# Kernel optimization log

Hardware: AMD Instinct MI355X
Metric: run time of the kernel (lower is better)

## Reference

```python
import jax, jax.numpy as jnp
import numpy as np

NUM_HEADS = 16
HEAD_DIM = 128
NUM_KV_HEADS = 8
NUM_KV_GROUPS = 2
HIDDEN = 2048
SCALE = 0.5  # hardcoded in the original SDPA call


def _fixed_sincos_pos(E, H):
    # matches ReusedProjReconstructor._fixed_sincos_pos (H even here)
    half = H // 2
    freq = jnp.exp(-jnp.log(jnp.float32(10000.0)) * jnp.arange(half, dtype=jnp.float32) / half)
    pos = jnp.arange(E, dtype=jnp.float32)[:, None]
    ang = pos * freq[None, :]
    return jnp.concatenate([jnp.sin(ang), jnp.cos(ang)], axis=1)  # [E, H]


def setup_inputs() -> dict:
    key = jax.random.key(0)
    ks = jax.random.split(key, 8)
    B, M, H = 4, 2048, HIDDEN
    kv_dim = NUM_KV_HEADS * HEAD_DIM
    s = 0.02
    return {
        "mem_act": jax.random.normal(ks[0], (B, M, H), jnp.float32),
        "Wq": jax.random.normal(ks[1], (H, H), jnp.float32) * s,
        "bq": jax.random.normal(ks[2], (H,), jnp.float32) * s,
        "Wk": jax.random.normal(ks[3], (kv_dim, H), jnp.float32) * s,
        "bk": jax.random.normal(ks[4], (kv_dim,), jnp.float32) * s,
        "Wv": jax.random.normal(ks[5], (kv_dim, H), jnp.float32) * s,
        "bv": jax.random.normal(ks[6], (kv_dim,), jnp.float32) * s,
        "Wo": jax.random.normal(ks[7], (H, H), jnp.float32) * s,
        "E": 2048,
    }


def reference(mem_act, Wq, bq, Wk, bk, Wv, bv, Wo, E):
    B, M, H = mem_act.shape
    # positional query hidden, shared across batch (q_ln is Identity)
    q_hidden = _fixed_sincos_pos(E, H).astype(mem_act.dtype)  # [E, H]
    q = (q_hidden @ Wq.T + bq).reshape(E, NUM_HEADS, HEAD_DIM)          # [E, nh, hd]
    k = (mem_act @ Wk.T + bk).reshape(B, M, NUM_KV_HEADS, HEAD_DIM)     # [B, M, nkv, hd]
    v = (mem_act @ Wv.T + bv).reshape(B, M, NUM_KV_HEADS, HEAD_DIM)
    # GQA: repeat kv heads (repeat_interleave over head dim)
    k = jnp.repeat(k, NUM_KV_GROUPS, axis=2)  # [B, M, nh, hd]
    v = jnp.repeat(v, NUM_KV_GROUPS, axis=2)
    # non-causal SDPA with scale=0.5, query broadcast over batch
    scores = jnp.einsum("ehd,bmhd->bhem", q, k) * SCALE  # [B, nh, E, M]
    attn = jax.nn.softmax(scores, axis=-1)
    out = jnp.einsum("bhem,bmhd->behd", attn, v).reshape(B, E, H)
    pred = out @ Wo.T  # o_proj (no bias, Qwen2 style)
    return pred
```

## Files before the change

### kernel.cpp

```cpp
#include <hip/hip_runtime.h>
#include <hip/hip_bf16.h>

typedef __attribute__((ext_vector_type(8))) short short8;
typedef __attribute__((ext_vector_type(4))) float f32x4;
typedef __attribute__((ext_vector_type(16))) float f32x16;
typedef unsigned short ushort_t;

__device__ __forceinline__ unsigned short f2bf(float x) {
    unsigned int u = __builtin_bit_cast(unsigned int, x);
    unsigned int r = (u + 0x7fffu + ((u >> 16) & 1u)) >> 16;
    return (unsigned short)r;
}

__device__ __forceinline__ void gload_lds16(const ushort_t* g, ushort_t* l) {
    __builtin_amdgcn_global_load_lds(
        (const __attribute__((address_space(1))) void*)g,
        (__attribute__((address_space(3))) void*)l, 16, 0, 0);
}

#define MFMA16(A, B, C) __builtin_amdgcn_mfma_f32_16x16x32_bf16((A), (B), (C), 0, 0, 0)
#define MFMA32(A, B, C) __builtin_amdgcn_mfma_f32_32x32x16_bf16((A), (B), (C), 0, 0, 0)

__global__ __launch_bounds__(256) void cvt_all(const float* __restrict__ im,
                                               const float* __restrict__ iq,
                                               const float* __restrict__ ik,
                                               const float* __restrict__ iv,
                                               const float* __restrict__ io,
                                               ushort_t* __restrict__ om,
                                               ushort_t* __restrict__ oq,
                                               ushort_t* __restrict__ ok,
                                               ushort_t* __restrict__ ov,
                                               ushort_t* __restrict__ oo) {
    long i = ((long)blockIdx.x * 256 + threadIdx.x) << 3;
    const float* s;
    ushort_t* d;
    if (i < 16777216)      { s = im + i;              d = om + i; }
    else if (i < 20971520) { s = iq + (i - 16777216); d = oq + (i - 16777216); }
    else if (i < 23068672) { s = ik + (i - 20971520); d = ok + (i - 20971520); }
    else if (i < 25165824) { s = iv + (i - 23068672); d = ov + (i - 23068672); }
    else                   { s = io + (i - 25165824); d = oo + (i - 25165824); }
    const float4* p = (const float4*)s;
    float4 a = p[0], b = p[1];
    short8 o;
    o[0] = (short)f2bf(a.x); o[1] = (short)f2bf(a.y);
    o[2] = (short)f2bf(a.z); o[3] = (short)f2bf(a.w);
    o[4] = (short)f2bf(b.x); o[5] = (short)f2bf(b.y);
    o[6] = (short)f2bf(b.z); o[7] = (short)f2bf(b.w);
    *(short8*)d = o;
}

__global__ __launch_bounds__(256) void fill_qh(ushort_t* __restrict__ qh) {
    int idx = blockIdx.x * 256 + threadIdx.x;
    int e = idx >> 10, i = idx & 1023;
    float freq = __expf(-9.2103403719761836f * (float)i * (1.0f / 1024.0f));
    float ang = (float)e * freq;
    qh[(size_t)e * 2048 + i]        = f2bf(sinf(ang));
    qh[(size_t)e * 2048 + 1024 + i] = f2bf(cosf(ang));
}

__global__ __launch_bounds__(256) void gemm_q(const ushort_t* __restrict__ A,
                                              const ushort_t* __restrict__ Bw,
                                              const float* __restrict__ bias,
                                              ushort_t* __restrict__ Cout,
                                              int M, int N, int K) {
    __shared__ ushort_t As[128 * 32];
    __shared__ ushort_t Bs[128 * 32];
    const int tid = threadIdx.x;
    const int lane = tid & 63;
    const int wid = tid >> 6;
    const int g = lane >> 4;
    const int r = lane & 15;
    const int wr = wid >> 1, wc = wid & 1;
    const int nbn = N >> 7;
    const int bm = blockIdx.x / nbn, bn = blockIdx.x % nbn;
    const int row0 = bm << 7, col0 = bn << 7;

    f32x4 acc[4][4];
#pragma unroll
    for (int i = 0; i < 4; ++i)
#pragma unroll
        for (int j = 0; j < 4; ++j) acc[i][j] = (f32x4){0.f, 0.f, 0.f, 0.f};

    const int f0 = tid * 8;
    const int r0_ = f0 >> 5, c0_ = f0 & 31;
    const int f1 = (256 + tid) * 8;
    const int r1_ = f1 >> 5, c1_ = f1 & 31;

    for (int k0 = 0; k0 < K; k0 += 32) {
        __syncthreads();
        gload_lds16(A  + (size_t)(row0 + r0_) * K + k0 + c0_, As + f0);
        gload_lds16(A  + (size_t)(row0 + r1_) * K + k0 + c1_, As + f1);
        gload_lds16(Bw + (size_t)(col0 + r0_) * K + k0 + c0_, Bs + f0);
        gload_lds16(Bw + (size_t)(col0 + r1_) * K + k0 + c1_, Bs + f1);
        __syncthreads();
        short8 af[4], bfr[4];
#pragma unroll
        for (int i = 0; i < 4; ++i) {
            af[i]  = *(const short8*)(As + (wr * 64 + i * 16 + r) * 32 + g * 8);
            bfr[i] = *(const short8*)(Bs + (wc * 64 + i * 16 + r) * 32 + g * 8);
        }
#pragma unroll
        for (int i = 0; i < 4; ++i)
#pragma unroll
            for (int j = 0; j < 4; ++j) acc[i][j] = MFMA16(af[i], bfr[j], acc[i][j]);
    }

#pragma unroll
    for (int j = 0; j < 4; ++j) {
        const int col = col0 + wc * 64 + j * 16 + r;
        const float bv = bias[col];
#pragma unroll
        for (int i = 0; i < 4; ++i) {
            const int rowb = row0 + wr * 64 + i * 16 + g * 4;
#pragma unroll
            for (int t = 0; t < 4; ++t) {
                float v = (acc[i][j][t] + bv) * 0.5f;
                Cout[(size_t)(rowb + t) * N + col] = f2bf(v);
            }
        }
    }
}

template <int EPI>
__global__ __launch_bounds__(512, 1) void gemm256(const ushort_t* __restrict__ A,
                                                  const ushort_t* __restrict__ Bw,
                                                  const float* __restrict__ b0,
                                                  const float* __restrict__ b1,
                                                  void* __restrict__ C0,
                                                  void* __restrict__ C1,
                                                  int M, int N, int K) {
    __shared__ ushort_t As[3][256 * 32];
    __shared__ ushort_t Bs[3][256 * 32];
    const int tid = threadIdx.x, lane = tid & 63;
    const int wid = tid >> 6;
    const int q5 = lane & 31, hi = lane >> 5;
    const int wm = wid >> 2, wn = wid & 3;
    const int nbn = N >> 8;
    const int nwg = gridDim.x;
    const int swz = (blockIdx.x & 7) * (nwg >> 3) + (blockIdx.x >> 3);
    const int bm = swz / nbn, bn = swz % nbn;
    const int row0 = bm << 8, col0 = bn << 8;
    const int NT = K >> 5;

    f32x16 acc[4][2];
#pragma unroll
    for (int mi = 0; mi < 4; ++mi)
#pragma unroll
        for (int nj = 0; nj < 2; ++nj)
#pragma unroll
            for (int rr = 0; rr < 16; ++rr) acc[mi][nj][rr] = 0.f;

    auto STAGE_HALF = [&](int buf, int kt, int i) {
        const int k0 = kt << 5;
        const int fb = (i * 512 + tid) << 4;
        const int rp = fb >> 7;
        const int bo = ((fb >> 4) & 7) ^ (rp & 7);
        const int row = rp * 2 + (bo >> 2);
        const int kc = (bo & 3) << 3;
        gload_lds16(A  + (size_t)(row0 + row) * K + k0 + kc, &As[buf][0] + (fb >> 1));
        gload_lds16(Bw + (size_t)(col0 + row) * K + k0 + kc, &Bs[buf][0] + (fb >> 1));
    };

    STAGE_HALF(0, 0, 0); STAGE_HALF(0, 0, 1);
    STAGE_HALF(1, 1, 0); STAGE_HALF(1, 1, 1);
    asm volatile("s_waitcnt vmcnt(4)" ::: "memory");
    __builtin_amdgcn_sched_barrier(0);
    __builtin_amdgcn_s_barrier();
    __builtin_amdgcn_sched_barrier(0);

    for (int t = 0; t < NT; ++t) {
        const int buf = t % 3;
        const char* Ab = (const char*)&As[buf][0];
        const char* Bb = (const char*)&Bs[buf][0];
#pragma unroll
        for (int ph = 0; ph < 2; ++ph) {
            short8 af[4], bfr[2];
#pragma unroll
            for (int nj = 0; nj < 2; ++nj) {
                const int col = wn * 64 + nj * 32 + q5;
                const int rp = col >> 1;
                const int blk = (((col & 1) << 2) + ph * 2 + hi) ^ (rp & 7);
                bfr[nj] = *(const short8*)(Bb + rp * 128 + blk * 16);
            }
#pragma unroll
            for (int mi = 0; mi < 4; ++mi) {
                const int row = wm * 128 + mi * 32 + q5;
                const int rp = row >> 1;
                const int blk = (((row & 1) << 2) + ph * 2 + hi) ^ (rp & 7);
                af[mi] = *(const short8*)(Ab + rp * 128 + blk * 16);
            }
            if (t + 2 < NT) STAGE_HALF((t + 2) % 3, t + 2, ph);
            __builtin_amdgcn_s_setprio(1);
#pragma unroll
            for (int mi = 0; mi < 4; ++mi)
#pragma unroll
                for (int nj = 0; nj < 2; ++nj)
                    acc[mi][nj] = MFMA32(af[mi], bfr[nj], acc[mi][nj]);
            __builtin_amdgcn_s_setprio(0);
            if (ph == 0) {
                __builtin_amdgcn_sched_barrier(0);
                __builtin_amdgcn_s_barrier();
                __builtin_amdgcn_sched_barrier(0);
            }
        }

        if (t + 2 < NT) {
            asm volatile("s_waitcnt vmcnt(4)" ::: "memory");
        } else if (t + 1 < NT) {
            asm volatile("s_waitcnt vmcnt(0)" ::: "memory");
        }
        if (t + 1 < NT) {
            __builtin_amdgcn_sched_barrier(0);
            __builtin_amdgcn_s_barrier();
            __builtin_amdgcn_sched_barrier(0);
        }
    }

#pragma unroll
    for (int mi = 0; mi < 4; ++mi)
#pragma unroll
        for (int nj = 0; nj < 2; ++nj) {
            const int col = col0 + wn * 64 + nj * 32 + q5;
            if (EPI == 2) {
                float* outp = (float*)C0;
#pragma unroll
                for (int rr = 0; rr < 16; ++rr) {
                    const int row = row0 + wm * 128 + mi * 32 + (rr & 3) + 8 * (rr >> 2) + 4 * hi;
                    outp[(size_t)row * N + col] = acc[mi][nj][rr];
                }
            } else {
                if (col < 1024) {
                    const float bv = b0[col];
                    ushort_t* Kp = (ushort_t*)C0;
#pragma unroll
                    for (int rr = 0; rr < 16; ++rr) {
                        const int row = row0 + wm * 128 + mi * 32 + (rr & 3) + 8 * (rr >> 2) + 4 * hi;
                        Kp[(size_t)row * 1024 + col] = f2bf(acc[mi][nj][rr] + bv);
                    }
                } else {
                    const int vcol = col - 1024;
                    const float bv = b1[vcol];
                    ushort_t* Vt = (ushort_t*)C1;
#pragma unroll
                    for (int G = 0; G < 4; ++G) {
                        const int m0 = row0 + wm * 128 + mi * 32 + G * 8 + 4 * hi;
                        const int bb = m0 >> 11;
                        const int mm = m0 & 2047;
                        const size_t vtrow = (size_t)(bb * 8 + (vcol >> 7)) * 128 + (vcol & 127);
                        unsigned int p0 = (unsigned int)f2bf(acc[mi][nj][G * 4 + 0] + bv)
                                        | ((unsigned int)f2bf(acc[mi][nj][G * 4 + 1] + bv) << 16);
                        unsigned int p1 = (unsigned int)f2bf(acc[mi][nj][G * 4 + 2] + bv)
                                        | ((unsigned int)f2bf(acc[mi][nj][G * 4 + 3] + bv) << 16);
                        uint2 pk; pk.x = p0; pk.y = p1;
                        *(uint2*)(Vt + vtrow * 2048 + mm) = pk;
                    }
                }
            }
        }
}

__global__ __launch_bounds__(512, 2) void attn_kernel(const ushort_t* __restrict__ Q,
                                                      const ushort_t* __restrict__ Kg,
                                                      const ushort_t* __restrict__ Vt,
                                                      ushort_t* __restrict__ O) {
    __shared__ ushort_t Ks[2][64 * 128];
    __shared__ ushort_t Vts[2][128 * 64];

    const int tid = threadIdx.x, lane = tid & 63, wid = tid >> 6;
    const int q5 = lane & 31;
    const int hi = lane >> 5;
    const int wq = wid & 3;
    const int wg = (blockIdx.x & 7) * 64 + (blockIdx.x >> 3);
    const int bkvh = wg >> 4;
    const int etile = wg & 15;
    const int b = bkvh >> 3, kvh = bkvh & 7;
    const int h = kvh * 2 + (wid >> 2);
    const int e0 = etile * 128;
    const int qrow = e0 + wq * 32 + q5;

    short8 Qf[8];
    {
        const ushort_t* qp = Q + (size_t)qrow * 2048 + h * 128 + hi * 8;
#pragma unroll
        for (int c = 0; c < 8; ++c) Qf[c] = *(const short8*)(qp + c * 16);
    }

    unsigned aK[2][8];
#pragma unroll
    for (int h2 = 0; h2 < 2; ++h2) {
        const int key = h2 * 32 + q5;
#pragma unroll
        for (int c = 0; c < 8; ++c)
            aK[h2][c] = key * 256 + (((c * 2 + hi) ^ (key & 7)) << 4);
    }
    unsigned aV[4];
#pragma unroll
    for (int c16 = 0; c16 < 4; ++c16)
        aV[c16] = q5 * 128 + (((c16 * 2 + hi) ^ (q5 & 7)) << 4);

    float lrow = 0.f;
    f32x16 oacc[4];
#pragma unroll
    for (int d0 = 0; d0 < 4; ++d0)
#pragma unroll
        for (int r = 0; r < 16; ++r) oacc[d0][r] = 0.f;

    f32x16 Z16;
#pragma unroll
    for (int r = 0; r < 16; ++r) Z16[r] = 0.f;

    const ushort_t* Kbase  = Kg + (size_t)b * 2048 * 1024 + kvh * 128;
    const ushort_t* Vtbase = Vt + (size_t)bkvh * 128 * 2048;

    auto STAGE = [&](int buf, int kv0) {
#pragma unroll
        for (int i = 0; i < 2; ++i) {
            const int fb = (i * 8 + wid) * 1024 + lane * 16;
            const int key = fb >> 8;
            const int blk = (fb >> 4) & 15;
            gload_lds16(Kbase + (size_t)(kv0 + key) * 1024 + ((blk ^ (key & 7)) << 3),
                        &Ks[buf][0] + (fb >> 1));
            const int d = fb >> 7;
            const int kb = (fb >> 4) & 7;
            gload_lds16(Vtbase + (size_t)d * 2048 + kv0 + ((kb ^ (d & 7)) << 3),
                        &Vts[buf][0] + (fb >> 1));
        }
    };

    auto TILE = [&](int bo) {
        f32x16 sS[2];
        __builtin_amdgcn_s_setprio(1);
#pragma unroll
        for (int c = 0; c < 8; ++c) {
            short8 ka0 = *(const short8*)((const char*)Ks + bo + aK[0][c]);
            short8 ka1 = *(const short8*)((const char*)Ks + bo + aK[1][c]);
            sS[0] = MFMA32(ka0, Qf[c], (c == 0) ? Z16 : sS[0]);
            sS[1] = MFMA32(ka1, Qf[c], (c == 0) ? Z16 : sS[1]);
        }
        __builtin_amdgcn_s_setprio(0);

#pragma unroll
        for (int h2 = 0; h2 < 2; ++h2)
#pragma unroll
            for (int r = 0; r < 16; ++r) sS[h2][r] = __expf(sS[h2][r]);

        float ts[16];
#pragma unroll
        for (int i = 0; i < 8; ++i) ts[i] = sS[0][2 * i] + sS[0][2 * i + 1];
#pragma unroll
        for (int i = 0; i < 8; ++i) ts[8 + i] = sS[1][2 * i] + sS[1][2 * i + 1];
#pragma unroll
        for (int s = 8; s > 0; s >>= 1)
#pragma unroll
            for (int i = 0; i < s; ++i) ts[i] += ts[i + s];
        lrow += ts[0] + __shfl_xor(ts[0], 32);

        unsigned int W[2][4][2];
#pragma unroll
        for (int h2 = 0; h2 < 2; ++h2)
#pragma unroll
            for (int q4 = 0; q4 < 4; ++q4)
#pragma unroll
                for (int p = 0; p < 2; ++p) {
                    unsigned int w;
                    asm("v_cvt_pk_bf16_f32 %0, %1, %2"
                        : "=v"(w)
                        : "v"(sS[h2][q4 * 4 + 2 * p]), "v"(sS[h2][q4 * 4 + 2 * p + 1]));
                    W[h2][q4][p] = w;
                }

#pragma unroll
        for (int c16 = 0; c16 < 4; ++c16) {
            const int h2 = c16 >> 1;
            const int q4a = (c16 & 1) * 2, q4b = q4a + 1;
            auto r0 = __builtin_amdgcn_permlane32_swap(W[h2][q4a][0], W[h2][q4b][0], false, false);
            auto r1 = __builtin_amdgcn_permlane32_swap(W[h2][q4a][1], W[h2][q4b][1], false, false);
            union { unsigned int w[4]; short8 v; } pa;
            pa.w[0] = r0[0];
            pa.w[1] = r1[0];
            pa.w[2] = r0[1];
            pa.w[3] = r1[1];
            __builtin_amdgcn_s_setprio(1);
#pragma unroll
            for (int d0 = 0; d0 < 4; ++d0) {
                short8 vb = *(const short8*)((const char*)Vts + bo + aV[c16] + d0 * 4096);
                oacc[d0] = MFMA32(pa.v, vb, oacc[d0]);
            }
            __builtin_amdgcn_s_setprio(0);
        }
    };

    STAGE(0, 0);
    __syncthreads();

#pragma unroll 1
    for (int tt = 0; tt < 16; ++tt) {
        STAGE(1, (2 * tt + 1) * 64);
        TILE(0);
        __syncthreads();
        if (tt < 15) STAGE(0, (2 * tt + 2) * 64);
        TILE(16384);
        __syncthreads();
    }

#pragma unroll
    for (int reg = 0; reg < 16; ++reg) {
        const int qr = (reg & 3) + 8 * (reg >> 2) + 4 * hi;
        const float lr = __shfl(lrow, qr);
        const float inv = 1.0f / lr;
        const int e = e0 + wq * 32 + qr;
        ushort_t* op = O + ((size_t)b * 2048 + e) * 2048 + h * 128 + q5;
#pragma unroll
        for (int d0 = 0; d0 < 4; ++d0)
            op[d0 * 32] = f2bf(oacc[d0][reg] * inv);
    }
}

extern "C" void kernel_launch(void* const* d_in, const int* in_sizes, int n_in,
                              void* d_out, int out_size, void* d_ws, size_t ws_size,
                              hipStream_t stream) {
    const float* mem_act = (const float*)d_in[0];
    const float* Wq = (const float*)d_in[1];
    const float* bq = (const float*)d_in[2];
    const float* Wk = (const float*)d_in[3];
    const float* bk = (const float*)d_in[4];
    const float* Wv = (const float*)d_in[5];
    const float* bv = (const float*)d_in[6];
    const float* Wo = (const float*)d_in[7];
    float* out = (float*)d_out;

    char* w = (char*)d_ws;
    ushort_t* memb = (ushort_t*)w; w += (size_t)16777216 * 2;
    ushort_t* wqb  = (ushort_t*)w; w += (size_t)4194304 * 2;
    ushort_t* wkvb = (ushort_t*)w; w += (size_t)4194304 * 2;
    ushort_t* wob  = (ushort_t*)w; w += (size_t)4194304 * 2;
    ushort_t* qh   = (ushort_t*)w; w += (size_t)4194304 * 2;
    ushort_t* Qp   = (ushort_t*)w; w += (size_t)4194304 * 2;
    ushort_t* Kp   = (ushort_t*)w; w += (size_t)8388608 * 2;
    ushort_t* Vtp  = (ushort_t*)w; w += (size_t)8388608 * 2;
    ushort_t* AO   = (ushort_t*)w; w += (size_t)16777216 * 2;

    dim3 blk(256);
    cvt_all<<<14336, blk, 0, stream>>>(mem_act, Wq, Wk, Wv, Wo,
                                       memb, wqb, wkvb, wkvb + (size_t)2097152, wob);
    fill_qh<<<(2048 * 1024) / 256, blk, 0, stream>>>(qh);

    gemm_q<<<16 * 16, blk, 0, stream>>>(qh, wqb, bq, Qp, 2048, 2048, 2048);

    gemm256<0><<<256, dim3(512), 0, stream>>>(memb, wkvb, bk, bv, Kp, Vtp, 8192, 2048, 2048);

    attn_kernel<<<512, dim3(512), 0, stream>>>(Qp, Kp, Vtp, AO);

    gemm256<2><<<256, dim3(512), 0, stream>>>(AO, wob, nullptr, nullptr, out, nullptr, 8192, 2048, 2048);
}
```

Before: 373.4 us.

## Shrink GEMM tiles to 256x128 with double buffering and fuse prep kernels

The large GEMMs move from 256x256 tiles with 512 threads, a triple-buffered LDS ring and one block per CU to 256x128 tiles with 256 threads, double buffering and up to three blocks per CU, launched as 512 blocks. The aim is more resident waves and better latency hiding across blocks, and with 256 CUs the doubled block count should fill the device better. In exchange the loads and barriers are coarser: each k-step waits for all loads with vmcnt(0). The fp32-to-bf16 conversion and sincos query fill are also merged into one launch to save a kernel launch.

```diff
diff --git a/kernel.cpp b/kernel.cpp
--- a/kernel.cpp
+++ b/kernel.cpp
@@ -21,41 +21,43 @@
 #define MFMA16(A, B, C) __builtin_amdgcn_mfma_f32_16x16x32_bf16((A), (B), (C), 0, 0, 0)
 #define MFMA32(A, B, C) __builtin_amdgcn_mfma_f32_32x32x16_bf16((A), (B), (C), 0, 0, 0)
 
-__global__ __launch_bounds__(256) void cvt_all(const float* __restrict__ im,
-                                               const float* __restrict__ iq,
-                                               const float* __restrict__ ik,
-                                               const float* __restrict__ iv,
-                                               const float* __restrict__ io,
-                                               ushort_t* __restrict__ om,
-                                               ushort_t* __restrict__ oq,
-                                               ushort_t* __restrict__ ok,
-                                               ushort_t* __restrict__ ov,
-                                               ushort_t* __restrict__ oo) {
-    long i = ((long)blockIdx.x * 256 + threadIdx.x) << 3;
-    const float* s;
-    ushort_t* d;
-    if (i < 16777216)      { s = im + i;              d = om + i; }
-    else if (i < 20971520) { s = iq + (i - 16777216); d = oq + (i - 16777216); }
-    else if (i < 23068672) { s = ik + (i - 20971520); d = ok + (i - 20971520); }
-    else if (i < 25165824) { s = iv + (i - 23068672); d = ov + (i - 23068672); }
-    else                   { s = io + (i - 25165824); d = oo + (i - 25165824); }
-    const float4* p = (const float4*)s;
-    float4 a = p[0], b = p[1];
-    short8 o;
-    o[0] = (short)f2bf(a.x); o[1] = (short)f2bf(a.y);
-    o[2] = (short)f2bf(a.z); o[3] = (short)f2bf(a.w);
-    o[4] = (short)f2bf(b.x); o[5] = (short)f2bf(b.y);
-    o[6] = (short)f2bf(b.z); o[7] = (short)f2bf(b.w);
-    *(short8*)d = o;
-}
-
-__global__ __launch_bounds__(256) void fill_qh(ushort_t* __restrict__ qh) {
-    int idx = blockIdx.x * 256 + threadIdx.x;
-    int e = idx >> 10, i = idx & 1023;
-    float freq = __expf(-9.2103403719761836f * (float)i * (1.0f / 1024.0f));
-    float ang = (float)e * freq;
-    qh[(size_t)e * 2048 + i]        = f2bf(sinf(ang));
-    qh[(size_t)e * 2048 + 1024 + i] = f2bf(cosf(ang));
+__global__ __launch_bounds__(256) void prep_all(const float* __restrict__ im,
+                                                const float* __restrict__ iq,
+                                                const float* __restrict__ ik,
+                                                const float* __restrict__ iv,
+                                                const float* __restrict__ io,
+                                                ushort_t* __restrict__ om,
+                                                ushort_t* __restrict__ oq,
+                                                ushort_t* __restrict__ ok,
+                                                ushort_t* __restrict__ ov,
+                                                ushort_t* __restrict__ oo,
+                                                ushort_t* __restrict__ qh) {
+    const int bid = blockIdx.x;
+    if (bid < 14336) {
+        long i = ((long)bid * 256 + threadIdx.x) << 3;
+        const float* s;
+        ushort_t* d;
+        if (i < 16777216)      { s = im + i;              d = om + i; }
+        else if (i < 20971520) { s = iq + (i - 16777216); d = oq + (i - 16777216); }
+        else if (i < 23068672) { s = ik + (i - 20971520); d = ok + (i - 20971520); }
+        else if (i < 25165824) { s = iv + (i - 23068672); d = ov + (i - 23068672); }
+        else                   { s = io + (i - 25165824); d = oo + (i - 25165824); }
+        const float4* p = (const float4*)s;
+        float4 a = p[0], b = p[1];
+        short8 o;
+        o[0] = (short)f2bf(a.x); o[1] = (short)f2bf(a.y);
+        o[2] = (short)f2bf(a.z); o[3] = (short)f2bf(a.w);
+        o[4] = (short)f2bf(b.x); o[5] = (short)f2bf(b.y);
+        o[6] = (short)f2bf(b.z); o[7] = (short)f2bf(b.w);
+        *(short8*)d = o;
+    } else {
+        int idx = (bid - 14336) * 256 + threadIdx.x;
+        int e = idx >> 10, i = idx & 1023;
+        float freq = __expf(-9.2103403719761836f * (float)i * (1.0f / 1024.0f));
+        float ang = (float)e * freq;
+        qh[(size_t)e * 2048 + i]        = f2bf(sinf(ang));
+        qh[(size_t)e * 2048 + 1024 + i] = f2bf(cosf(ang));
+    }
 }
 
 __global__ __launch_bounds__(256) void gemm_q(const ushort_t* __restrict__ A,
@@ -122,24 +124,24 @@
 }
 
 template <int EPI>
-__global__ __launch_bounds__(512, 1) void gemm256(const ushort_t* __restrict__ A,
-                                                  const ushort_t* __restrict__ Bw,
-                                                  const float* __restrict__ b0,
-                                                  const float* __restrict__ b1,
-                                                  void* __restrict__ C0,
-                                                  void* __restrict__ C1,
-                                                  int M, int N, int K) {
-    __shared__ ushort_t As[3][256 * 32];
-    __shared__ ushort_t Bs[3][256 * 32];
+__global__ __launch_bounds__(256, 3) void gemm256b(const ushort_t* __restrict__ A,
+                                                   const ushort_t* __restrict__ Bw,
+                                                   const float* __restrict__ b0,
+                                                   const float* __restrict__ b1,
+                                                   void* __restrict__ C0,
+                                                   void* __restrict__ C1,
+                                                   int M, int N, int K) {
+    __shared__ ushort_t As[2][256 * 32];
+    __shared__ ushort_t Bs[2][128 * 32];
     const int tid = threadIdx.x, lane = tid & 63;
     const int wid = tid >> 6;
     const int q5 = lane & 31, hi = lane >> 5;
-    const int wm = wid >> 2, wn = wid & 3;
-    const int nbn = N >> 8;
+    const int wm = wid >> 1, wn = wid & 1;
+    const int nbn = N >> 7;
     const int nwg = gridDim.x;
     const int swz = (blockIdx.x & 7) * (nwg >> 3) + (blockIdx.x >> 3);
     const int bm = swz / nbn, bn = swz % nbn;
-    const int row0 = bm << 8, col0 = bn << 8;
+    const int row0 = bm << 8, col0 = bn << 7;
     const int NT = K >> 5;
 
     f32x16 acc[4][2];
@@ -150,26 +152,32 @@
 #pragma unroll
             for (int rr = 0; rr < 16; ++rr) acc[mi][nj][rr] = 0.f;
 
-    auto STAGE_HALF = [&](int buf, int kt, int i) {
-        const int k0 = kt << 5;
-        const int fb = (i * 512 + tid) << 4;
+    auto STAGE_A = [&](int buf, int kt, int i) {
+        const int fb = (i * 256 + tid) << 4;
         const int rp = fb >> 7;
         const int bo = ((fb >> 4) & 7) ^ (rp & 7);
         const int row = rp * 2 + (bo >> 2);
         const int kc = (bo & 3) << 3;
-        gload_lds16(A  + (size_t)(row0 + row) * K + k0 + kc, &As[buf][0] + (fb >> 1));
-        gload_lds16(Bw + (size_t)(col0 + row) * K + k0 + kc, &Bs[buf][0] + (fb >> 1));
+        gload_lds16(A + (size_t)(row0 + row) * K + (kt << 5) + kc, &As[buf][0] + (fb >> 1));
     };
-
-    STAGE_HALF(0, 0, 0); STAGE_HALF(0, 0, 1);
-    STAGE_HALF(1, 1, 0); STAGE_HALF(1, 1, 1);
-    asm volatile("s_waitcnt vmcnt(4)" ::: "memory");
+    auto STAGE_B = [&](int buf, int kt, int i) {
+        const int fb = (i * 256 + tid) << 4;
+        const int rp = fb >> 7;
+        const int bo = ((fb >> 4) & 7) ^ (rp & 7);
+        const int row = rp * 2 + (bo >> 2);
+        const int kc = (bo & 3) << 3;
+        gload_lds16(Bw + (size_t)(col0 + row) * K + (kt << 5) + kc, &Bs[buf][0] + (fb >> 1));
+    };
+
+    STAGE_A(0, 0, 0); STAGE_A(0, 0, 1); STAGE_A(0, 0, 2); STAGE_A(0, 0, 3);
+    STAGE_B(0, 0, 0); STAGE_B(0, 0, 1);
+    asm volatile("s_waitcnt vmcnt(0)" ::: "memory");
     __builtin_amdgcn_sched_barrier(0);
     __builtin_amdgcn_s_barrier();
     __builtin_amdgcn_sched_barrier(0);
 
     for (int t = 0; t < NT; ++t) {
-        const int buf = t % 3;
+        const int buf = t & 1;
         const char* Ab = (const char*)&As[buf][0];
         const char* Bb = (const char*)&Bs[buf][0];
 #pragma unroll
@@ -189,7 +197,11 @@
                 const int blk = (((row & 1) << 2) + ph * 2 + hi) ^ (rp & 7);
                 af[mi] = *(const short8*)(Ab + rp * 128 + blk * 16);
             }
-            if (t + 2 < NT) STAGE_HALF((t + 2) % 3, t + 2, ph);
+            if (t + 1 < NT) {
+                STAGE_A(buf ^ 1, t + 1, ph * 2);
+                STAGE_A(buf ^ 1, t + 1, ph * 2 + 1);
+                STAGE_B(buf ^ 1, t + 1, ph);
+            }
             __builtin_amdgcn_s_setprio(1);
 #pragma unroll
             for (int mi = 0; mi < 4; ++mi)
@@ -197,19 +209,10 @@
                 for (int nj = 0; nj < 2; ++nj)
                     acc[mi][nj] = MFMA32(af[mi], bfr[nj], acc[mi][nj]);
             __builtin_amdgcn_s_setprio(0);
-            if (ph == 0) {
-                __builtin_amdgcn_sched_barrier(0);
-                __builtin_amdgcn_s_barrier();
-                __builtin_amdgcn_sched_barrier(0);
-            }
-        }
-
-        if (t + 2 < NT) {
-            asm volatile("s_waitcnt vmcnt(4)" ::: "memory");
-        } else if (t + 1 < NT) {
+        }
+
+        if (t + 1 < NT) {
             asm volatile("s_waitcnt vmcnt(0)" ::: "memory");
-        }
-        if (t + 1 < NT) {
             __builtin_amdgcn_sched_barrier(0);
             __builtin_amdgcn_s_barrier();
             __builtin_amdgcn_sched_barrier(0);
@@ -441,15 +444,14 @@
     ushort_t* AO   = (ushort_t*)w; w += (size_t)16777216 * 2;
 
     dim3 blk(256);
-    cvt_all<<<14336, blk, 0, stream>>>(mem_act, Wq, Wk, Wv, Wo,
-                                       memb, wqb, wkvb, wkvb + (size_t)2097152, wob);
-    fill_qh<<<(2048 * 1024) / 256, blk, 0, stream>>>(qh);
+    prep_all<<<22528, blk, 0, stream>>>(mem_act, Wq, Wk, Wv, Wo,
+                                        memb, wqb, wkvb, wkvb + (size_t)2097152, wob, qh);
 
     gemm_q<<<16 * 16, blk, 0, stream>>>(qh, wqb, bq, Qp, 2048, 2048, 2048);
 
-    gemm256<0><<<256, dim3(512), 0, stream>>>(memb, wkvb, bk, bv, Kp, Vtp, 8192, 2048, 2048);
+    gemm256b<0><<<512, blk, 0, stream>>>(memb, wkvb, bk, bv, Kp, Vtp, 8192, 2048, 2048);
 
     attn_kernel<<<512, dim3(512), 0, stream>>>(Qp, Kp, Vtp, AO);
 
-    gemm256<2><<<256, dim3(512), 0, stream>>>(AO, wob, nullptr, nullptr, out, nullptr, 8192, 2048, 2048);
-}
+    gemm256b<2><<<512, blk, 0, stream>>>(AO, wob, nullptr, nullptr, out, nullptr, 8192, 2048, 2048);
+}
```

New measurement: 441.7 us. +18.3%, slower.

## Deepen GEMM LDS pipeline to four stages and merge prep kernels

Applied to the files above, without the earlier changes.

The 256x256 GEMM now uses four LDS buffers instead of three and prefetches three K-tiles ahead. This allows the mid-iteration barrier between the two phases to be removed, so there is only one barrier per K-tile. The fp32-to-bf16 conversion and the sinusoidal query fill are merged into one launch to save a kernel launch. The cost is more LDS per block (128KB), which could lower occupancy; the launch bounds already force one block per CU, so that is likely tolerable.

```diff
diff --git a/kernel.cpp b/kernel.cpp
--- a/kernel.cpp
+++ b/kernel.cpp
@@ -21,41 +21,43 @@
 #define MFMA16(A, B, C) __builtin_amdgcn_mfma_f32_16x16x32_bf16((A), (B), (C), 0, 0, 0)
 #define MFMA32(A, B, C) __builtin_amdgcn_mfma_f32_32x32x16_bf16((A), (B), (C), 0, 0, 0)
 
-__global__ __launch_bounds__(256) void cvt_all(const float* __restrict__ im,
-                                               const float* __restrict__ iq,
-                                               const float* __restrict__ ik,
-                                               const float* __restrict__ iv,
-                                               const float* __restrict__ io,
-                                               ushort_t* __restrict__ om,
-                                               ushort_t* __restrict__ oq,
-                                               ushort_t* __restrict__ ok,
-                                               ushort_t* __restrict__ ov,
-                                               ushort_t* __restrict__ oo) {
-    long i = ((long)blockIdx.x * 256 + threadIdx.x) << 3;
-    const float* s;
-    ushort_t* d;
-    if (i < 16777216)      { s = im + i;              d = om + i; }
-    else if (i < 20971520) { s = iq + (i - 16777216); d = oq + (i - 16777216); }
-    else if (i < 23068672) { s = ik + (i - 20971520); d = ok + (i - 20971520); }
-    else if (i < 25165824) { s = iv + (i - 23068672); d = ov + (i - 23068672); }
-    else                   { s = io + (i - 25165824); d = oo + (i - 25165824); }
-    const float4* p = (const float4*)s;
-    float4 a = p[0], b = p[1];
-    short8 o;
-    o[0] = (short)f2bf(a.x); o[1] = (short)f2bf(a.y);
-    o[2] = (short)f2bf(a.z); o[3] = (short)f2bf(a.w);
-    o[4] = (short)f2bf(b.x); o[5] = (short)f2bf(b.y);
-    o[6] = (short)f2bf(b.z); o[7] = (short)f2bf(b.w);
-    *(short8*)d = o;
-}
-
-__global__ __launch_bounds__(256) void fill_qh(ushort_t* __restrict__ qh) {
-    int idx = blockIdx.x * 256 + threadIdx.x;
-    int e = idx >> 10, i = idx & 1023;
-    float freq = __expf(-9.2103403719761836f * (float)i * (1.0f / 1024.0f));
-    float ang = (float)e * freq;
-    qh[(size_t)e * 2048 + i]        = f2bf(sinf(ang));
-    qh[(size_t)e * 2048 + 1024 + i] = f2bf(cosf(ang));
+__global__ __launch_bounds__(256) void prep_all(const float* __restrict__ im,
+                                                const float* __restrict__ iq,
+                                                const float* __restrict__ ik,
+                                                const float* __restrict__ iv,
+                                                const float* __restrict__ io,
+                                                ushort_t* __restrict__ om,
+                                                ushort_t* __restrict__ oq,
+                                                ushort_t* __restrict__ ok,
+                                                ushort_t* __restrict__ ov,
+                                                ushort_t* __restrict__ oo,
+                                                ushort_t* __restrict__ qh) {
+    const int bid = blockIdx.x;
+    if (bid < 14336) {
+        long i = ((long)bid * 256 + threadIdx.x) << 3;
+        const float* s;
+        ushort_t* d;
+        if (i < 16777216)      { s = im + i;              d = om + i; }
+        else if (i < 20971520) { s = iq + (i - 16777216); d = oq + (i - 16777216); }
+        else if (i < 23068672) { s = ik + (i - 20971520); d = ok + (i - 20971520); }
+        else if (i < 25165824) { s = iv + (i - 23068672); d = ov + (i - 23068672); }
+        else                   { s = io + (i - 25165824); d = oo + (i - 25165824); }
+        const float4* p = (const float4*)s;
+        float4 a = p[0], b = p[1];
+        short8 o;
+        o[0] = (short)f2bf(a.x); o[1] = (short)f2bf(a.y);
+        o[2] = (short)f2bf(a.z); o[3] = (short)f2bf(a.w);
+        o[4] = (short)f2bf(b.x); o[5] = (short)f2bf(b.y);
+        o[6] = (short)f2bf(b.z); o[7] = (short)f2bf(b.w);
+        *(short8*)d = o;
+    } else {
+        int idx = (bid - 14336) * 256 + threadIdx.x;
+        int e = idx >> 10, i = idx & 1023;
+        float freq = __expf(-9.2103403719761836f * (float)i * (1.0f / 1024.0f));
+        float ang = (float)e * freq;
+        qh[(size_t)e * 2048 + i]        = f2bf(sinf(ang));
+        qh[(size_t)e * 2048 + 1024 + i] = f2bf(cosf(ang));
+    }
 }
 
 __global__ __launch_bounds__(256) void gemm_q(const ushort_t* __restrict__ A,
@@ -129,8 +131,8 @@
                                                   void* __restrict__ C0,
                                                   void* __restrict__ C1,
                                                   int M, int N, int K) {
-    __shared__ ushort_t As[3][256 * 32];
-    __shared__ ushort_t Bs[3][256 * 32];
+    __shared__ ushort_t As[4][256 * 32];
+    __shared__ ushort_t Bs[4][256 * 32];
     const int tid = threadIdx.x, lane = tid & 63;
     const int wid = tid >> 6;
     const int q5 = lane & 31, hi = lane >> 5;
@@ -163,13 +165,14 @@
 
     STAGE_HALF(0, 0, 0); STAGE_HALF(0, 0, 1);
     STAGE_HALF(1, 1, 0); STAGE_HALF(1, 1, 1);
-    asm volatile("s_waitcnt vmcnt(4)" ::: "memory");
+    STAGE_HALF(2, 2, 0); STAGE_HALF(2, 2, 1);
+    asm volatile("s_waitcnt vmcnt(8)" ::: "memory");
     __builtin_amdgcn_sched_barrier(0);
     __builtin_amdgcn_s_barrier();
     __builtin_amdgcn_sched_barrier(0);
 
     for (int t = 0; t < NT; ++t) {
-        const int buf = t % 3;
+        const int buf = t & 3;
         const char* Ab = (const char*)&As[buf][0];
         const char* Bb = (const char*)&Bs[buf][0];
 #pragma unroll
@@ -189,7 +192,7 @@
                 const int blk = (((row & 1) << 2) + ph * 2 + hi) ^ (rp & 7);
                 af[mi] = *(const short8*)(Ab + rp * 128 + blk * 16);
             }
-            if (t + 2 < NT) STAGE_HALF((t + 2) % 3, t + 2, ph);
+            if (t + 3 < NT) STAGE_HALF((t + 3) & 3, t + 3, ph);
             __builtin_amdgcn_s_setprio(1);
 #pragma unroll
             for (int mi = 0; mi < 4; ++mi)
@@ -197,14 +200,11 @@
                 for (int nj = 0; nj < 2; ++nj)
                     acc[mi][nj] = MFMA32(af[mi], bfr[nj], acc[mi][nj]);
             __builtin_amdgcn_s_setprio(0);
-            if (ph == 0) {
-                __builtin_amdgcn_sched_barrier(0);
-                __builtin_amdgcn_s_barrier();
-                __builtin_amdgcn_sched_barrier(0);
-            }
-        }
-
-        if (t + 2 < NT) {
+        }
+
+        if (t + 3 < NT) {
+            asm volatile("s_waitcnt vmcnt(8)" ::: "memory");
+        } else if (t + 2 < NT) {
             asm volatile("s_waitcnt vmcnt(4)" ::: "memory");
         } else if (t + 1 < NT) {
             asm volatile("s_waitcnt vmcnt(0)" ::: "memory");
@@ -441,9 +441,8 @@
     ushort_t* AO   = (ushort_t*)w; w += (size_t)16777216 * 2;
 
     dim3 blk(256);
-    cvt_all<<<14336, blk, 0, stream>>>(mem_act, Wq, Wk, Wv, Wo,
-                                       memb, wqb, wkvb, wkvb + (size_t)2097152, wob);
-    fill_qh<<<(2048 * 1024) / 256, blk, 0, stream>>>(qh);
+    prep_all<<<22528, blk, 0, stream>>>(mem_act, Wq, Wk, Wv, Wo,
+                                        memb, wqb, wkvb, wkvb + (size_t)2097152, wob, qh);
 
     gemm_q<<<16 * 16, blk, 0, stream>>>(qh, wqb, bq, Qp, 2048, 2048, 2048);
 
```

After: 367.8 us. No clear change (-1.5%).
